# Performance work log

Hardware: AMD Instinct MI355X
Metric: run time of the kernel (lower is better)

Reference implementation:

```python
import jax, jax.numpy as jnp
import numpy as np

B, S, L = 32, 50, 16            # batch, seq_len, lectures per step
C, D = 50, 64                   # num_concepts, hidden_dim (key=value=summary dim)
NQ, NL, NU = 10000, 2000, 5000  # num_items, num_nonassessed_items, num_users
QV = NQ + NL + 1                # q_embed vocab (questions + lectures + pad)
QAV = 2 * NQ + 1                # qa_embed vocab
H4 = 4 * D                      # linear_dim = 4 * value_dim
EPS = 1e-5                      # torch LayerNorm default eps


def setup_inputs() -> dict:
    ks = jax.random.split(jax.random.key(0), 16)
    rn = lambda k, sh, sc: jax.random.normal(k, sh, jnp.float32) * sc
    return dict(
        q_data=jax.random.randint(ks[0], (B, S), 0, QV),
        qa_data=jax.random.randint(ks[1], (B, S), 0, QAV),
        l_data=jax.random.randint(ks[2], (B, S, L), 0, QV),
        users=jax.random.randint(ks[3], (B,), 0, NU + 1),
        key_matrix=rn(ks[4], (C, D), (2.0 / D) ** 0.5),   # key_matrix_embed rows 1..C (kaiming)
        q_embed=rn(ks[5], (QV, D), 0.02),
        qa_embed=rn(ks[6], (QAV, D), 0.02),
        u_embed=rn(ks[7], (NU + 1, D), 0.02),             # looked up but unused by write()
        M0=rn(ks[8], (C, D), (2.0 / D) ** 0.5),           # kaiming-init value matrix
        W_e=rn(ks[9], (D, D), D ** -0.5), b_e=jnp.zeros((D,), jnp.float32),
        W_a=rn(ks[10], (D, D), D ** -0.5), b_a=jnp.zeros((D,), jnp.float32),
        ln_gamma=jnp.ones((H4,), jnp.float32), ln_beta=jnp.zeros((H4,), jnp.float32),
        W0=rn(ks[11], (H4, H4), H4 ** -0.5), b0=jnp.zeros((H4,), jnp.float32),
        W1=rn(ks[12], (H4, H4), H4 ** -0.5), b1=jnp.zeros((H4,), jnp.float32),
        W_out=rn(ks[13], (H4, 1), H4 ** -0.5), b_out=jnp.zeros((1,), jnp.float32),
    )


def _forward(q_data, qa_data, l_data, key_matrix, q_embed, qa_embed, M0,
             W_e, b_e, W_a, b_a, ln_gamma, ln_beta, W0, b0, W1, b1, W_out, b_out):
    Bv = q_data.shape[0]
    q_e = q_embed[q_data]        # (B,S,D)
    qa_e = qa_embed[qa_data]     # (B,S,D)
    l_e = q_embed[l_data]        # (B,S,L,D) lectures share the q embedding table

    corr = lambda x: jax.nn.softmax(x @ key_matrix.T, axis=-1)  # softmax addressing
    q_cw = corr(q_e)             # (B,S,C)
    l_cw = corr(l_e)             # (B,S,L,C)
    # erase / add gates are memory-independent -> precompute (batched GEMMs)
    l_er = jax.nn.sigmoid(l_e @ W_e + b_e); l_ad = jnp.tanh(l_e @ W_a + b_a)
    q_er = jax.nn.sigmoid(qa_e @ W_e + b_e); q_ad = jnp.tanh(qa_e @ W_a + b_a)

    tm2 = lambda x: jnp.swapaxes(x, 0, 1)           # (B,S,..) -> (S,B,..)
    tm3 = lambda x: jnp.transpose(x, (1, 2, 0, 3))  # (B,S,L,..) -> (S,L,B,..)
    xs = (tm2(q_cw), tm2(q_e), tm2(q_er), tm2(q_ad),
          tm3(l_cw), tm3(l_e), tm3(l_er), tm3(l_ad))

    def write(M, w, e, a):  # erase-add gated write
        w = w[:, :, None]   # (B,C,1)
        return M * (1.0 - w * e[:, None, :]) + w * a[:, None, :]

    def layer_norm(x):
        mu = jnp.mean(x, -1, keepdims=True)
        v = jnp.var(x, -1, keepdims=True)
        return (x - mu) * jax.lax.rsqrt(v + EPS) * ln_gamma + ln_beta

    def outer(M, step):
        qcw, q, qer, qad, lcw, le, ler, lad = step
        q_read = jnp.einsum('bc,bcd->bd', qcw, M)  # read BEFORE lecture writes

        def inner(carry, lx):
            Mc, acc = carry
            w, e, a = lx
            acc = acc + jnp.einsum('bc,bcd->bd', w, Mc)  # read then write
            return (write(Mc, w, e, a), acc), None

        (M, l_read), _ = jax.lax.scan(inner, (M, jnp.zeros_like(q)), (lcw, ler, lad))
        # `l` after the loop is the LAST lecture embedding of this step
        mastery = layer_norm(jnp.concatenate([q_read, q, l_read, le[-1]], axis=-1))
        h = jax.nn.relu(mastery @ W0 + b0) @ W1 + b1   # dropout = identity (eval)
        pred = jax.nn.sigmoid(h @ W_out + b_out)[:, 0]
        M = write(M, qcw, qer, qad)                    # commit the q/a interaction
        return M, pred

    M_init = jnp.broadcast_to(M0, (Bv,) + M0.shape)
    _, preds = jax.lax.scan(outer, M_init, xs)
    return jnp.swapaxes(preds, 0, 1)                   # (B,S)


def reference(q_data, qa_data, l_data, users, key_matrix, q_embed, qa_embed,
              u_embed, M0, W_e, b_e, W_a, b_a, ln_gamma, ln_beta,
              W0, b0, W1, b1, W_out, b_out):
    # users/u_embed are looked up by the torch module but unused by write()'s math
    return _forward(q_data, qa_data, l_data, key_matrix, q_embed, qa_embed, M0,
                    W_e, b_e, W_a, b_a, ln_gamma, ln_beta, W0, b0, W1, b1, W_out, b_out)
```

## Files before the change

### kernel.cpp

```cpp
#include <hip/hip_runtime.h>
#include <math.h>

#define BB 32
#define SS 50
#define LL 16
#define CC 50
#define DD 64
#define NCH 13
#define H4 256
#define NROWS_Q (BB*SS)
#define NROWS_L (BB*SS*LL)

#define EA_ST 2304
#define W_ST  68

#define RB 64
#define NBLK_L (NROWS_L/RB)
#define NBLK_Q (NROWS_Q/RB)
#define NGB (NBLK_L + 2*NBLK_Q)

#define KBAT 16
#define NBAT (H4/KBAT)

static_assert(EA_ST == 17*128 + 128, "ea record: 17 slots x 64 lanes x float2, +pad");
static_assert(W_ST == 17*4, "w record: 17 slots x 4 chunk-cols");
static_assert(SS % 2 == 0, "phaseA double-step pipeline needs even SS");
static_assert(NROWS_L % RB == 0 && NROWS_Q % RB == 0, "GEMM row blocking");
static_assert(NBAT*KBAT == H4 && NBAT % 2 == 0,
              "phaseB k-loop must cover ALL of H4 in pairs of batches");

#define OFF_EA     ((size_t)0)
#define OFF_W      (OFF_EA + (size_t)NROWS_Q*EA_ST)
#define OFF_PQ     (OFF_W  + (size_t)BB*NCH*SS*W_ST)
#define OFF_PL     (OFF_PQ + (size_t)NROWS_Q*DD)
#define OFF_QE     (OFF_PL + (size_t)NROWS_Q*DD)
#define OFF_LELAST (OFF_QE + (size_t)NROWS_Q*DD)

__global__ __launch_bounds__(256, 4) void k0_kernel(
    const int* __restrict__ qd, const int* __restrict__ qadx,
    const int* __restrict__ ld,
    const float* __restrict__ Kmat, const float* __restrict__ qemb,
    const float* __restrict__ qaemb,
    const float* __restrict__ We, const float* __restrict__ Wa,
    const float* __restrict__ be, const float* __restrict__ ba,
    float* __restrict__ eaW, float* __restrict__ wrecW,
    float* __restrict__ Pzero,
    float* __restrict__ q_e_o, float* __restrict__ le_last)
{
    __shared__ float sX[RB*DD];
    __shared__ float sW[32*192];

    int tid = threadIdx.x;
    int bid = blockIdx.x;

    for (int i = bid*256 + tid; i < 2*NROWS_Q*DD; i += NGB*256) Pzero[i] = 0.f;

    int bt, base;
    if (bid < NBLK_L)              { bt = 0; base = bid*RB; }
    else if (bid < NBLK_L+NBLK_Q)  { bt = 1; base = (bid-NBLK_L)*RB; }
    else                           { bt = 2; base = (bid-NBLK_L-NBLK_Q)*RB; }

    {
        const int*   idsrc = (bt==0) ? ld : (bt==1) ? qd : qadx;
        const float* tab   = (bt==2) ? qaemb : qemb;
        for (int idx = tid; idx < RB*16; idx += 256) {
            int r = idx >> 4, q = idx & 15;
            int id = idsrc[base + r];
            *(float4*)(sX + r*64 + q*4) =
                *(const float4*)(tab + (size_t)id*DD + q*4);
        }
    }

    auto stageW = [&](int kb) {
        #pragma unroll
        for (int n = 0; n < 4; ++n) {
            int f  = n*256 + tid;
            int kl = f >> 5, cf = f & 31;
            int k  = kb + kl;
            const float* src = (cf < 16) ? (We + k*64 + cf*4)
                                         : (Wa + k*64 + (cf-16)*4);
            *(float4*)(sW + kl*192 + cf*4) = *(const float4*)src;
        }
        #pragma unroll
        for (int n = 0; n < 8; ++n) {
            int f  = n*256 + tid;
            int kl = f >> 6, cr = f & 63;
            int k  = kb + kl;
            sW[kl*192 + 128 + cr] = (cr < CC) ? Kmat[cr*64 + k] : 0.f;
        }
    };

    int lane = tid & 63, wvi = tid >> 6;
    int r0 = wvi * 16;

    float accE[16], accA[16], accS[16];
    #pragma unroll
    for (int r = 0; r < 16; ++r) { accE[r] = 0.f; accA[r] = 0.f; accS[r] = 0.f; }

    stageW(0);
    __syncthreads();

    #pragma unroll 2
    for (int k4 = 0; k4 < 8; ++k4) {
        float wE[4], wA4[4], wS[4];
        #pragma unroll
        for (int kk = 0; kk < 4; ++kk) {
            int krow = (k4*4 + kk)*192;
            wE[kk]  = sW[krow + lane];
            wA4[kk] = sW[krow + 64 + lane];
            wS[kk]  = sW[krow + 128 + lane];
        }
        #pragma unroll
        for (int r = 0; r < 16; ++r) {
            float4 xv = *(const float4*)(sX + (r0+r)*64 + k4*4);
            accE[r] = fmaf(xv.x, wE[0], accE[r]);
            accE[r] = fmaf(xv.y, wE[1], accE[r]);
            accE[r] = fmaf(xv.z, wE[2], accE[r]);
            accE[r] = fmaf(xv.w, wE[3], accE[r]);
            accA[r] = fmaf(xv.x, wA4[0], accA[r]);
            accA[r] = fmaf(xv.y, wA4[1], accA[r]);
            accA[r] = fmaf(xv.z, wA4[2], accA[r]);
            accA[r] = fmaf(xv.w, wA4[3], accA[r]);
            accS[r] = fmaf(xv.x, wS[0], accS[r]);
            accS[r] = fmaf(xv.y, wS[1], accS[r]);
            accS[r] = fmaf(xv.z, wS[2], accS[r]);
            accS[r] = fmaf(xv.w, wS[3], accS[r]);
        }
    }
    __syncthreads();

    stageW(32);
    __syncthreads();

    #pragma unroll 2
    for (int k4 = 0; k4 < 8; ++k4) {
        float wE[4], wA4[4], wS[4];
        #pragma unroll
        for (int kk = 0; kk < 4; ++kk) {
            int krow = (k4*4 + kk)*192;
            wE[kk]  = sW[krow + lane];
            wA4[kk] = sW[krow + 64 + lane];
            wS[kk]  = sW[krow + 128 + lane];
        }
        #pragma unroll
        for (int r = 0; r < 16; ++r) {
            float4 xv = *(const float4*)(sX + (r0+r)*64 + 32 + k4*4);
            accE[r] = fmaf(xv.x, wE[0], accE[r]);
            accE[r] = fmaf(xv.y, wE[1], accE[r]);
            accE[r] = fmaf(xv.z, wE[2], accE[r]);
            accE[r] = fmaf(xv.w, wE[3], accE[r]);
            accA[r] = fmaf(xv.x, wA4[0], accA[r]);
            accA[r] = fmaf(xv.y, wA4[1], accA[r]);
            accA[r] = fmaf(xv.z, wA4[2], accA[r]);
            accA[r] = fmaf(xv.w, wA4[3], accA[r]);
            accS[r] = fmaf(xv.x, wS[0], accS[r]);
            accS[r] = fmaf(xv.y, wS[1], accS[r]);
            accS[r] = fmaf(xv.z, wS[2], accS[r]);
            accS[r] = fmaf(xv.w, wS[3], accS[r]);
        }
    }

    float bev = be[lane], bav = ba[lane];

    #pragma unroll
    for (int r = 0; r < 16; ++r) {
        int rr = r0 + r;
        int grow = base + rr;

        float s = (lane < CC) ? accS[r] : -1e30f;
        float mx = s;
        #pragma unroll
        for (int o = 32; o >= 1; o >>= 1) mx = fmaxf(mx, __shfl_xor(mx, o));
        float p = (lane < CC) ? expf(s - mx) : 0.f;
        float sum = p;
        #pragma unroll
        for (int o = 32; o >= 1; o >>= 1) sum += __shfl_xor(sum, o);
        float wsm = p / sum;

        if (bt == 0) {
            float erv = 1.f / (1.f + expf(-(accE[r] + bev)));
            float adv = tanhf(accA[r] + bav);
            int bs = grow >> 4, il = grow & 15;
            *(float2*)(eaW + (size_t)bs*EA_ST + il*128 + lane*2) =
                make_float2(erv, adv);
            int b = bs / SS, s2 = bs - b*SS;
            if (lane < 52) {
                int omx = lane >> 2, j = lane & 3;
                wrecW[(((size_t)(b*NCH + omx)*SS + s2)*17 + il)*4 + j] =
                    (lane < CC) ? wsm : 0.f;
            }
            if (il == LL-1) le_last[(size_t)bs*DD + lane] = sX[rr*64 + lane];
        } else if (bt == 1) {
            int qrow = grow;
            int b = qrow / SS, s2 = qrow - b*SS;
            if (lane < 52) {
                int omx = lane >> 2, j = lane & 3;
                wrecW[(((size_t)(b*NCH + omx)*SS + s2)*17 + 16)*4 + j] =
                    (lane < CC) ? wsm : 0.f;
            }
            q_e_o[(size_t)qrow*DD + lane] = sX[rr*64 + lane];
        } else {
            float erv = 1.f / (1.f + expf(-(accE[r] + bev)));
            float adv = tanhf(accA[r] + bav);
            int qrow = grow;
            *(float2*)(eaW + (size_t)qrow*EA_ST + 2048 + lane*2) =
                make_float2(erv, adv);
        }
    }
}

__global__ __launch_bounds__(64) void phaseA_kernel(
    const float* __restrict__ M0,
    const float* __restrict__ ea, const float* __restrict__ wrec,
    float* __restrict__ Pq, float* __restrict__ Pl)
{
    int om   = blockIdx.x >> 5;
    int b    = blockIdx.x & 31;
    int lane = threadIdx.x;
    int c0   = om * 4;

    __shared__ __align__(16) float wbuf[2][W_ST];

    float M[4];
    #pragma unroll
    for (int i = 0; i < 4; ++i) {
        int c = c0 + i;
        M[i] = (c < CC) ? M0[c*DD + lane] : 0.f;
    }

    const float* eb = ea   + (size_t)b*SS*EA_ST + lane*2;
    const float* wb = wrec + (size_t)(b*NCH + om)*SS*W_ST;
    float* pq = Pq + (size_t)b*SS*DD + lane;
    float* pl = Pl + (size_t)b*SS*DD + lane;

    float2 ea0[17], ea1[17];

    #pragma unroll
    for (int il = 0; il < 17; ++il)
        ea0[il] = *(const float2*)(eb + il*128);
    if (lane < 17)
        *(float4*)&wbuf[0][lane*4] = *(const float4*)(wb + lane*4);

    auto step = [&](int s, float2 (&cur)[17], float2 (&nxt)[17], int wbsel) {
        bool pf = (s < SS-1);
        float4 rw;
        if (pf) {
            const float* eg = eb + (size_t)(s+1)*EA_ST;
            #pragma unroll
            for (int il = 0; il < 17; ++il)
                nxt[il] = *(const float2*)(eg + il*128);
            if (lane < 17)
                rw = *(const float4*)(wb + (size_t)(s+1)*W_ST + lane*4);
        }

        float4 qw = *(const float4*)&wbuf[wbsel][64];
        float qr;
        qr = qw.x * M[0];
        qr = fmaf(qw.y, M[1], qr);
        qr = fmaf(qw.z, M[2], qr);
        qr = fmaf(qw.w, M[3], qr);

        float a0 = 0.f, a1 = 0.f, a2 = 0.f, a3 = 0.f;
        #pragma unroll
        for (int il = 0; il < 16; ++il) {
            float4 w = *(const float4*)&wbuf[wbsel][il*4];
            float e = cur[il].x, a = cur[il].y;
            a0 = fmaf(w.x, M[0], a0);
            a1 = fmaf(w.y, M[1], a1);
            a2 = fmaf(w.z, M[2], a2);
            a3 = fmaf(w.w, M[3], a3);
            M[0] = fmaf(w.x, fmaf(-e, M[0], a), M[0]);
            M[1] = fmaf(w.y, fmaf(-e, M[1], a), M[1]);
            M[2] = fmaf(w.z, fmaf(-e, M[2], a), M[2]);
            M[3] = fmaf(w.w, fmaf(-e, M[3], a), M[3]);
        }

        atomicAdd(pq + (size_t)s*DD, qr);
        atomicAdd(pl + (size_t)s*DD, (a0 + a1) + (a2 + a3));

        {
            float e = cur[16].x, a = cur[16].y;
            M[0] = fmaf(qw.x, fmaf(-e, M[0], a), M[0]);
            M[1] = fmaf(qw.y, fmaf(-e, M[1], a), M[1]);
            M[2] = fmaf(qw.z, fmaf(-e, M[2], a), M[2]);
            M[3] = fmaf(qw.w, fmaf(-e, M[3], a), M[3]);
        }

        if (pf && lane < 17)
            *(float4*)&wbuf[wbsel ^ 1][lane*4] = rw;
    };

    for (int s = 0; s < SS; s += 2) {
        step(s,     ea0, ea1, 0);
        step(s + 1, ea1, ea0, 1);
    }
}

__global__ __launch_bounds__(256) void phaseB_kernel(
    const float* __restrict__ Pq, const float* __restrict__ Pl,
    const float* __restrict__ q_e_i, const float* __restrict__ le_last,
    const float* __restrict__ ln_g, const float* __restrict__ ln_b,
    const float* __restrict__ W0, const float* __restrict__ b0,
    const float* __restrict__ W1, const float* __restrict__ b1,
    const float* __restrict__ Wout, const float* __restrict__ bout,
    float* __restrict__ out)
{
    __shared__ float m[8][H4];
    __shared__ float h[8][H4];
    __shared__ float red[8][4];

    int j = threadIdx.x;
    int g0 = blockIdx.x * 8;
    int lane = j & 63, wv = j >> 6;

    int seg = j >> 6, dd = j & 63;
    #pragma unroll
    for (int r = 0; r < 8; ++r) {
        int g = g0 + r;
        float v;
        if      (seg == 0) v = Pq[(size_t)g*DD + dd];
        else if (seg == 1) v = q_e_i[(size_t)g*DD + dd];
        else if (seg == 2) v = Pl[(size_t)g*DD + dd];
        else               v = le_last[(size_t)g*DD + dd];
        m[r][j] = v;
    }
    __syncthreads();

    #pragma unroll
    for (int rr = 0; rr < 2; ++rr) {
        int r = wv + rr*4;
        float4 v4 = *(((const float4*)&m[r][0]) + lane);
        float s1 = v4.x + v4.y + v4.z + v4.w;
        float s2 = v4.x*v4.x + v4.y*v4.y + v4.z*v4.z + v4.w*v4.w;
        #pragma unroll
        for (int o = 32; o >= 1; o >>= 1) {
            s1 += __shfl_xor(s1, o);
            s2 += __shfl_xor(s2, o);
        }
        float mu  = s1 * (1.f/256.f);
        float var = s2 * (1.f/256.f) - mu*mu;
        float is  = rsqrtf(var + 1e-5f);
        float4 g4 = *(((const float4*)ln_g) + lane);
        float4 b4 = *(((const float4*)ln_b) + lane);
        float4 o4;
        o4.x = (v4.x - mu)*is*g4.x + b4.x;
        o4.y = (v4.y - mu)*is*g4.y + b4.y;
        o4.z = (v4.z - mu)*is*g4.z + b4.z;
        o4.w = (v4.w - mu)*is*g4.w + b4.w;
        *(((float4*)&m[r][0]) + lane) = o4;
    }
    __syncthreads();

    const float* Wp = W0 + j;
    float acc[8];
    {
        float bj = b0[j];
        #pragma unroll
        for (int r = 0; r < 8; ++r) acc[r] = bj;
    }
    {
        float wA[KBAT], wB[KBAT];
        #pragma unroll
        for (int t = 0; t < KBAT; ++t) wA[t] = Wp[(size_t)t*H4];
        #pragma unroll 1
        for (int kb = 0; kb < NBAT; kb += 2) {
            #pragma unroll
            for (int t = 0; t < KBAT; ++t)
                wB[t] = Wp[(size_t)((kb+1)*KBAT + t)*H4];
            #pragma unroll
            for (int t4 = 0; t4 < KBAT/4; ++t4) {
                #pragma unroll
                for (int r = 0; r < 8; ++r) {
                    float4 mv = *(const float4*)&m[r][kb*KBAT + t4*4];
                    acc[r] = fmaf(mv.x, wA[t4*4+0], acc[r]);
                    acc[r] = fmaf(mv.y, wA[t4*4+1], acc[r]);
                    acc[r] = fmaf(mv.z, wA[t4*4+2], acc[r]);
                    acc[r] = fmaf(mv.w, wA[t4*4+3], acc[r]);
                }
            }
            if (kb + 2 < NBAT) {
                #pragma unroll
                for (int t = 0; t < KBAT; ++t)
                    wA[t] = Wp[(size_t)((kb+2)*KBAT + t)*H4];
            }
            #pragma unroll
            for (int t4 = 0; t4 < KBAT/4; ++t4) {
                #pragma unroll
                for (int r = 0; r < 8; ++r) {
                    float4 mv = *(const float4*)&m[r][(kb+1)*KBAT + t4*4];
                    acc[r] = fmaf(mv.x, wB[t4*4+0], acc[r]);
                    acc[r] = fmaf(mv.y, wB[t4*4+1], acc[r]);
                    acc[r] = fmaf(mv.z, wB[t4*4+2], acc[r]);
                    acc[r] = fmaf(mv.w, wB[t4*4+3], acc[r]);
                }
            }
        }
    }
    #pragma unroll
    for (int r = 0; r < 8; ++r) h[r][j] = fmaxf(acc[r], 0.f);
    __syncthreads();

    const float* Wp1 = W1 + j;
    float a2[8];
    {
        float bj = b1[j];
        #pragma unroll
        for (int r = 0; r < 8; ++r) a2[r] = bj;
    }
    {
        float wA[KBAT], wB[KBAT];
        #pragma unroll
        for (int t = 0; t < KBAT; ++t) wA[t] = Wp1[(size_t)t*H4];
        #pragma unroll 1
        for (int kb = 0; kb < NBAT; kb += 2) {
            #pragma unroll
            for (int t = 0; t < KBAT; ++t)
                wB[t] = Wp1[(size_t)((kb+1)*KBAT + t)*H4];
            #pragma unroll
            for (int t4 = 0; t4 < KBAT/4; ++t4) {
                #pragma unroll
                for (int r = 0; r < 8; ++r) {
                    float4 hv = *(const float4*)&h[r][kb*KBAT + t4*4];
                    a2[r] = fmaf(hv.x, wA[t4*4+0], a2[r]);
                    a2[r] = fmaf(hv.y, wA[t4*4+1], a2[r]);
                    a2[r] = fmaf(hv.z, wA[t4*4+2], a2[r]);
                    a2[r] = fmaf(hv.w, wA[t4*4+3], a2[r]);
                }
            }
            if (kb + 2 < NBAT) {
                #pragma unroll
                for (int t = 0; t < KBAT; ++t)
                    wA[t] = Wp1[(size_t)((kb+2)*KBAT + t)*H4];
            }
            #pragma unroll
            for (int t4 = 0; t4 < KBAT/4; ++t4) {
                #pragma unroll
                for (int r = 0; r < 8; ++r) {
                    float4 hv = *(const float4*)&h[r][(kb+1)*KBAT + t4*4];
                    a2[r] = fmaf(hv.x, wB[t4*4+0], a2[r]);
                    a2[r] = fmaf(hv.y, wB[t4*4+1], a2[r]);
                    a2[r] = fmaf(hv.z, wB[t4*4+2], a2[r]);
                    a2[r] = fmaf(hv.w, wB[t4*4+3], a2[r]);
                }
            }
        }
    }

    float wo = Wout[j];
    #pragma unroll
    for (int r = 0; r < 8; ++r) {
        float v = a2[r] * wo;
        #pragma unroll
        for (int o = 32; o >= 1; o >>= 1) v += __shfl_xor(v, o);
        if (lane == 0) red[r][wv] = v;
    }
    __syncthreads();
    if (j < 8) {
        float t = red[j][0] + red[j][1] + red[j][2] + red[j][3] + bout[0];
        out[g0 + j] = 1.f / (1.f + expf(-t));
    }
}

extern "C" void kernel_launch(void* const* d_in, const int* in_sizes, int n_in,
                              void* d_out, int out_size, void* d_ws, size_t ws_size,
                              hipStream_t stream)
{
    const int*   q_data  = (const int*)  d_in[0];
    const int*   qa_data = (const int*)  d_in[1];
    const int*   l_data  = (const int*)  d_in[2];
    const float* Kmat    = (const float*)d_in[4];
    const float* q_embed = (const float*)d_in[5];
    const float* qa_embed= (const float*)d_in[6];
    const float* M0      = (const float*)d_in[8];
    const float* W_e     = (const float*)d_in[9];
    const float* b_e     = (const float*)d_in[10];
    const float* W_a     = (const float*)d_in[11];
    const float* b_a     = (const float*)d_in[12];
    const float* ln_g    = (const float*)d_in[13];
    const float* ln_b    = (const float*)d_in[14];
    const float* W0      = (const float*)d_in[15];
    const float* b0      = (const float*)d_in[16];
    const float* W1      = (const float*)d_in[17];
    const float* b1      = (const float*)d_in[18];
    const float* W_out   = (const float*)d_in[19];
    const float* b_out   = (const float*)d_in[20];

    float* ws = (float*)d_ws;
    float* eaW     = ws + OFF_EA;
    float* wrecW   = ws + OFF_W;
    float* Pq      = ws + OFF_PQ;
    float* Pl      = ws + OFF_PL;
    float* q_e     = ws + OFF_QE;
    float* le_last = ws + OFF_LELAST;

    float* out = (float*)d_out;

    k0_kernel<<<NGB, 256, 0, stream>>>(q_data, qa_data, l_data,
                                       Kmat, q_embed, qa_embed,
                                       W_e, W_a, b_e, b_a,
                                       eaW, wrecW, Pq,
                                       q_e, le_last);
    phaseA_kernel<<<BB*NCH, 64, 0, stream>>>(M0, eaW, wrecW, Pq, Pl);
    phaseB_kernel<<<NROWS_Q/8, 256, 0, stream>>>(Pq, Pl, q_e, le_last,
                                                 ln_g, ln_b, W0, b0, W1, b1,
                                                 W_out, b_out, out);
}
```

Baseline: 206.6 us.

## Replace phaseA global atomics with per-chunk partial buffers reduced in phaseB

PhaseA no longer atomically adds each step's read contributions into shared global Pq/Pl. Each block buffers its partials in LDS and copies them out with float4 stores to a per-chunk slot, and phaseB sums the 13 chunk partials when it loads. This removes the zero-fill pass in k0 and the atomic traffic on the serial recurrence path. In exchange phaseB does more global reads, phaseA uses about 25KB of LDS per 64-thread block, and the ea record padding is dropped, which may change bank or channel behaviour.

Result: faster. 199.4 us (-3.5%).

```diff
diff --git a/kernel.cpp b/kernel.cpp
--- a/kernel.cpp
+++ b/kernel.cpp
@@ -11,7 +11,7 @@
 #define NROWS_Q (BB*SS)
 #define NROWS_L (BB*SS*LL)
 
-#define EA_ST 2304
+#define EA_ST 2176
 #define W_ST  68
 
 #define RB 64
@@ -22,18 +22,19 @@
 #define KBAT 16
 #define NBAT (H4/KBAT)
 
-static_assert(EA_ST == 17*128 + 128, "ea record: 17 slots x 64 lanes x float2, +pad");
+static_assert(EA_ST == 17*128, "ea record: 17 slots x 64 lanes x float2");
 static_assert(W_ST == 17*4, "w record: 17 slots x 4 chunk-cols");
 static_assert(SS % 2 == 0, "phaseA double-step pipeline needs even SS");
 static_assert(NROWS_L % RB == 0 && NROWS_Q % RB == 0, "GEMM row blocking");
 static_assert(NBAT*KBAT == H4 && NBAT % 2 == 0,
               "phaseB k-loop must cover ALL of H4 in pairs of batches");
+static_assert(SS*DD % 4 == 0, "phaseA partial copy uses float4");
 
 #define OFF_EA     ((size_t)0)
 #define OFF_W      (OFF_EA + (size_t)NROWS_Q*EA_ST)
-#define OFF_PQ     (OFF_W  + (size_t)BB*NCH*SS*W_ST)
-#define OFF_PL     (OFF_PQ + (size_t)NROWS_Q*DD)
-#define OFF_QE     (OFF_PL + (size_t)NROWS_Q*DD)
+#define OFF_PQP    (OFF_W  + (size_t)BB*NCH*SS*W_ST)
+#define OFF_PLP    (OFF_PQP + (size_t)NCH*BB*SS*DD)
+#define OFF_QE     (OFF_PLP + (size_t)NCH*BB*SS*DD)
 #define OFF_LELAST (OFF_QE + (size_t)NROWS_Q*DD)
 
 __global__ __launch_bounds__(256, 4) void k0_kernel(
@@ -44,7 +45,6 @@
     const float* __restrict__ We, const float* __restrict__ Wa,
     const float* __restrict__ be, const float* __restrict__ ba,
     float* __restrict__ eaW, float* __restrict__ wrecW,
-    float* __restrict__ Pzero,
     float* __restrict__ q_e_o, float* __restrict__ le_last)
 {
     __shared__ float sX[RB*DD];
@@ -52,8 +52,6 @@
 
     int tid = threadIdx.x;
     int bid = blockIdx.x;
-
-    for (int i = bid*256 + tid; i < 2*NROWS_Q*DD; i += NGB*256) Pzero[i] = 0.f;
 
     int bt, base;
     if (bid < NBLK_L)              { bt = 0; base = bid*RB; }
@@ -212,7 +210,7 @@
 __global__ __launch_bounds__(64) void phaseA_kernel(
     const float* __restrict__ M0,
     const float* __restrict__ ea, const float* __restrict__ wrec,
-    float* __restrict__ Pq, float* __restrict__ Pl)
+    float* __restrict__ PqP, float* __restrict__ PlP)
 {
     int om   = blockIdx.x >> 5;
     int b    = blockIdx.x & 31;
@@ -220,6 +218,8 @@
     int c0   = om * 4;
 
     __shared__ __align__(16) float wbuf[2][W_ST];
+    __shared__ __align__(16) float sPq[SS*DD];
+    __shared__ __align__(16) float sPl[SS*DD];
 
     float M[4];
     #pragma unroll
@@ -230,8 +230,6 @@
 
     const float* eb = ea   + (size_t)b*SS*EA_ST + lane*2;
     const float* wb = wrec + (size_t)(b*NCH + om)*SS*W_ST;
-    float* pq = Pq + (size_t)b*SS*DD + lane;
-    float* pl = Pl + (size_t)b*SS*DD + lane;
 
     float2 ea0[17], ea1[17];
 
@@ -275,8 +273,8 @@
             M[3] = fmaf(w.w, fmaf(-e, M[3], a), M[3]);
         }
 
-        atomicAdd(pq + (size_t)s*DD, qr);
-        atomicAdd(pl + (size_t)s*DD, (a0 + a1) + (a2 + a3));
+        sPq[s*DD + lane] = qr;
+        sPl[s*DD + lane] = (a0 + a1) + (a2 + a3);
 
         {
             float e = cur[16].x, a = cur[16].y;
@@ -294,10 +292,17 @@
         step(s,     ea0, ea1, 0);
         step(s + 1, ea1, ea0, 1);
     }
+
+    float* pqo = PqP + (size_t)(om*BB + b)*SS*DD;
+    float* plo = PlP + (size_t)(om*BB + b)*SS*DD;
+    for (int f = lane; f < SS*DD/4; f += 64) {
+        *(float4*)(pqo + f*4) = *(const float4*)(sPq + f*4);
+        *(float4*)(plo + f*4) = *(const float4*)(sPl + f*4);
+    }
 }
 
 __global__ __launch_bounds__(256) void phaseB_kernel(
-    const float* __restrict__ Pq, const float* __restrict__ Pl,
+    const float* __restrict__ PqP, const float* __restrict__ PlP,
     const float* __restrict__ q_e_i, const float* __restrict__ le_last,
     const float* __restrict__ ln_g, const float* __restrict__ ln_b,
     const float* __restrict__ W0, const float* __restrict__ b0,
@@ -318,10 +323,21 @@
     for (int r = 0; r < 8; ++r) {
         int g = g0 + r;
         float v;
-        if      (seg == 0) v = Pq[(size_t)g*DD + dd];
-        else if (seg == 1) v = q_e_i[(size_t)g*DD + dd];
-        else if (seg == 2) v = Pl[(size_t)g*DD + dd];
-        else               v = le_last[(size_t)g*DD + dd];
+        if (seg == 0) {
+            v = 0.f;
+            #pragma unroll
+            for (int om = 0; om < NCH; ++om)
+                v += PqP[((size_t)om*BB*SS + g)*DD + dd];
+        } else if (seg == 1) {
+            v = q_e_i[(size_t)g*DD + dd];
+        } else if (seg == 2) {
+            v = 0.f;
+            #pragma unroll
+            for (int om = 0; om < NCH; ++om)
+                v += PlP[((size_t)om*BB*SS + g)*DD + dd];
+        } else {
+            v = le_last[(size_t)g*DD + dd];
+        }
         m[r][j] = v;
     }
     __syncthreads();
@@ -488,8 +504,8 @@
     float* ws = (float*)d_ws;
     float* eaW     = ws + OFF_EA;
     float* wrecW   = ws + OFF_W;
-    float* Pq      = ws + OFF_PQ;
-    float* Pl      = ws + OFF_PL;
+    float* PqP     = ws + OFF_PQP;
+    float* PlP     = ws + OFF_PLP;
     float* q_e     = ws + OFF_QE;
     float* le_last = ws + OFF_LELAST;
 
@@ -498,10 +514,10 @@
     k0_kernel<<<NGB, 256, 0, stream>>>(q_data, qa_data, l_data,
                                        Kmat, q_embed, qa_embed,
                                        W_e, W_a, b_e, b_a,
-                                       eaW, wrecW, Pq,
+                                       eaW, wrecW,
                                        q_e, le_last);
-    phaseA_kernel<<<BB*NCH, 64, 0, stream>>>(M0, eaW, wrecW, Pq, Pl);
-    phaseB_kernel<<<NROWS_Q/8, 256, 0, stream>>>(Pq, Pl, q_e, le_last,
+    phaseA_kernel<<<BB*NCH, 64, 0, stream>>>(M0, eaW, wrecW, PqP, PlP);
+    phaseB_kernel<<<NROWS_Q/8, 256, 0, stream>>>(PqP, PlP, q_e, le_last,
                                                  ln_g, ln_b, W0, b0, W1, b1,
                                                  W_out, b_out, out);
 }
```
